# Kernel tuning notes

Hardware: AMD Instinct MI355X
Metric: run time of the kernel (lower is better)

## Reference

```python
import jax, jax.numpy as jnp
import numpy as np

NUM_EXPERTS = 8
TOP_K = 2


def setup_inputs() -> dict:
    key = jax.random.key(0)
    k1, k2, k3, k4 = jax.random.split(key, 4)
    B, T, C, E, D = 4, 2048, 2048, NUM_EXPERTS, 2048
    scale = 0.02
    return {
        "x": jax.random.normal(k1, (B, T, C), dtype=jnp.float32),
        "w_router": jax.random.normal(k2, (C, E), dtype=jnp.float32) * scale,
        "w_fc": jax.random.normal(k3, (E, C, D), dtype=jnp.float32) * scale,
        "w_proj": jax.random.normal(k4, (E, D, C), dtype=jnp.float32) * scale,
    }


def reference(x, w_router, w_fc, w_proj):
    B, T, C = x.shape
    E = w_fc.shape[0]
    x_flat = x.reshape(-1, C)                       # [N, C]
    N = x_flat.shape[0]

    router_logits = x_flat @ w_router                # [N, E]
    top_vals, top_idx = jax.lax.top_k(router_logits, TOP_K)  # [N, K]
    probs = jax.nn.softmax(top_vals, axis=-1)        # [N, K]

    # Per-token combine weight for each expert (0 if not selected).
    rows = jnp.arange(N)[:, None]                    # [N, 1]
    w_tok = jnp.zeros((N, E), dtype=x.dtype).at[rows, top_idx].add(probs)  # [N, E]

    # Dense grouped computation over experts (same math as masked loop):
    # hidden = relu(x W_fc)^2, then project and combine with routing weights.
    h = jnp.einsum('nc,ecd->ned', x_flat, w_fc)      # [N, E, D]
    h = jnp.square(jax.nn.relu(h))
    y = jnp.einsum('ned,edc->nec', h, w_proj)        # [N, E, C]
    out = jnp.einsum('nec,ne->nc', y, w_tok)         # [N, C]
    return out.reshape(B, T, C)
```

## Files before the change

kernel.cpp:

```cpp
#include <hip/hip_runtime.h>

typedef float   f32x4 __attribute__((ext_vector_type(4)));
typedef _Float16 f16x8 __attribute__((ext_vector_type(8)));
typedef short   s16x8 __attribute__((ext_vector_type(8)));
typedef short   s16x4 __attribute__((ext_vector_type(4)));
typedef unsigned short u16;

#define NTOK 8192
#define CDIM 2048
#define NEXP 8
#define NASS 16384
#define MTILES 24

#define GLOBAL_AS __attribute__((address_space(1)))
#define LDS_AS    __attribute__((address_space(3)))

__device__ __forceinline__ u16 f2h_bits(float f) {
  _Float16 h = (_Float16)f;
  union { _Float16 h; u16 u; } v;
  v.h = h;
  return v.u;
}

__global__ __launch_bounds__(256) void moe_wrt(
    const float* __restrict__ wr, float* __restrict__ wrT)
{
  const int gid = blockIdx.x * 256 + threadIdx.x;
  const int c = gid >> 3, e = gid & 7;
  wrT[e * CDIM + c] = wr[c * NEXP + e];
}

__global__ __launch_bounds__(256) void moe_router(
    const float* __restrict__ x, const float* __restrict__ wrT,
    u16* __restrict__ xh, int* __restrict__ top_idx,
    float* __restrict__ top_p, int* __restrict__ counts)
{
  const int wave = threadIdx.x >> 6, lane = threadIdx.x & 63;
  const int n = blockIdx.x * 4 + wave;
  const float* xr = x + (size_t)n * CDIM;
  u16* xhr = xh + (size_t)n * CDIM;
  float acc[NEXP] = {};
  #pragma unroll
  for (int i = 0; i < CDIM / 256; ++i) {
    const int c = i * 256 + lane * 4;
    const f32x4 xv = *(const f32x4*)(xr + c);
    s16x4 hv;
    #pragma unroll
    for (int j = 0; j < 4; ++j) hv[j] = (short)f2h_bits(xv[j]);
    *(s16x4*)(xhr + c) = hv;
    #pragma unroll
    for (int e = 0; e < NEXP; ++e) {
      const f32x4 wv = *(const f32x4*)(wrT + (size_t)e * CDIM + c);
      acc[e] += xv[0]*wv[0] + xv[1]*wv[1] + xv[2]*wv[2] + xv[3]*wv[3];
    }
  }
  #pragma unroll
  for (int off = 32; off > 0; off >>= 1) {
    #pragma unroll
    for (int e = 0; e < NEXP; ++e) acc[e] += __shfl_xor(acc[e], off);
  }
  if (lane == 0) {
    int i0 = 0; float v0 = acc[0];
    #pragma unroll
    for (int e = 1; e < NEXP; ++e) { if (acc[e] > v0) { v0 = acc[e]; i0 = e; } }
    int i1 = -1; float v1 = -3.4e38f;
    #pragma unroll
    for (int e = 0; e < NEXP; ++e) { if (e != i0 && acc[e] > v1) { v1 = acc[e]; i1 = e; } }
    const float ex = __expf(v1 - v0);
    const float p0 = 1.f / (1.f + ex);
    top_idx[n * 2 + 0] = i0; top_idx[n * 2 + 1] = i1;
    top_p[n * 2 + 0] = p0;   top_p[n * 2 + 1] = 1.f - p0;
    atomicAdd(&counts[i0], 1);
    atomicAdd(&counts[i1], 1);
  }
}

__global__ void moe_offsets(const int* __restrict__ counts,
                            int* __restrict__ offs, int* __restrict__ fill)
{
  if (threadIdx.x == 0) {
    int s = 0;
    for (int e = 0; e < NEXP; ++e) { offs[e] = s; fill[e] = s; s += counts[e]; }
    offs[NEXP] = s;
  }
}

__global__ __launch_bounds__(256) void moe_scatter(
    const int* __restrict__ top_idx, const float* __restrict__ top_p,
    int* fill, int* __restrict__ tok_s, float* __restrict__ prb_s)
{
  const int n = blockIdx.x * 256 + threadIdx.x;
  #pragma unroll
  for (int k = 0; k < 2; ++k) {
    const int e = top_idx[n * 2 + k];
    const int pos = atomicAdd(&fill[e], 1);
    tok_s[pos] = n;
    prb_s[pos] = top_p[n * 2 + k];
  }
}

__global__ __launch_bounds__(256) void moe_transpose(
    const float* __restrict__ wfc, const float* __restrict__ wpj,
    u16* __restrict__ wfcT, u16* __restrict__ wpjT)
{
  const float* src = blockIdx.z ? wpj : wfc;
  u16* dst = blockIdx.z ? wpjT : wfcT;
  const int e = blockIdx.y;
  src += (size_t)e * CDIM * CDIM;
  dst += (size_t)e * CDIM * CDIM;
  const int tr = (blockIdx.x >> 5) * 64;
  const int tc = (blockIdx.x & 31) * 64;
  __shared__ float lds[64][65];
  const int t = threadIdx.x;
  #pragma unroll
  for (int p = 0; p < 4; ++p) {
    const int r  = p * 16 + (t >> 4);
    const int c4 = (t & 15) * 4;
    const f32x4 v = *(const f32x4*)(src + (size_t)(tr + r) * CDIM + tc + c4);
    #pragma unroll
    for (int j = 0; j < 4; ++j) lds[r][c4 + j] = v[j];
  }
  __syncthreads();
  const int d  = t >> 2;
  const int cs = (t & 3) * 16;
  s16x8 o0, o1;
  #pragma unroll
  for (int j = 0; j < 8; ++j) o0[j] = (short)f2h_bits(lds[cs + j][d]);
  #pragma unroll
  for (int j = 0; j < 8; ++j) o1[j] = (short)f2h_bits(lds[cs + 8 + j][d]);
  u16* drow = dst + (size_t)(tc + d) * CDIM + tr + cs;
  *(s16x8*)(drow + 0) = o0;
  *(s16x8*)(drow + 8) = o1;
}

template<int MODE>
__global__ __launch_bounds__(512, 4) void moe_gemm8(
    const u16* __restrict__ A, const u16* __restrict__ W,
    const int* __restrict__ tok_s, const float* __restrict__ prb_s,
    const int* __restrict__ offs, u16* __restrict__ hout,
    float* __restrict__ out)
{
  const int id    = blockIdx.x;
  const int nt    = id & 7;
  const int rid   = id >> 3;
  const int e     = rid / MTILES;
  const int mtile = rid % MTILES;
  const int off0  = offs[e];
  const int Me    = offs[e + 1] - off0;
  const int m0    = mtile * 128;
  if (m0 >= Me) return;
  const int n0 = nt * 256;
  const u16* We = W + (size_t)e * CDIM * CDIM;

  __shared__ u16 As[3][128 * 32];
  __shared__ u16 Bs[3][256 * 32];

  const int t    = threadIdx.x;
  const int lane = t & 63, wv = t >> 6;
  const int wm = wv >> 2, wn = wv & 3;

  const int l     = lane;
  const int kchnk = (l & 3) ^ ((l >> 3) & 3);
  const int kelem = kchnk * 8;
  const int rloc  = 2 * (l >> 3) + ((l >> 2) & 1);
  const int rA  = wv * 16 + rloc;
  const int mrA = m0 + rA;
  const int rrA = (mrA < Me) ? mrA : (Me - 1);
  const int gaA = (MODE == 0) ? tok_s[off0 + rrA] : (off0 + rrA);
  const u16* asrc = A + (size_t)gaA * CDIM + kelem;
  const int rB0 = wv * 32 + rloc;
  const int rB1 = wv * 32 + 16 + rloc;
  const u16* bsrc0 = We + (size_t)(n0 + rB0) * CDIM + kelem;
  const u16* bsrc1 = We + (size_t)(n0 + rB1) * CDIM + kelem;

  #define STAGE(T_, bb_)                                                       \
    { const int kk_ = (T_) * 32;                                               \
      __builtin_amdgcn_global_load_lds(                                        \
          (const GLOBAL_AS void*)(asrc + kk_),                                 \
          (LDS_AS void*)&As[bb_][wv * 512], 16, 0, 0);                         \
      __builtin_amdgcn_global_load_lds(                                        \
          (const GLOBAL_AS void*)(bsrc0 + kk_),                                \
          (LDS_AS void*)&Bs[bb_][wv * 1024], 16, 0, 0);                        \
      __builtin_amdgcn_global_load_lds(                                        \
          (const GLOBAL_AS void*)(bsrc1 + kk_),                                \
          (LDS_AS void*)&Bs[bb_][wv * 1024 + 512], 16, 0, 0); }

  const int rsel     = lane & 15;
  const int g        = lane >> 4;
  const int halfline = rsel >> 1;
  const int slotx    = (((rsel & 1) * 4) + (g ^ (halfline & 3))) * 8;

  f32x4 acc[4][4] = {};

  #define COMPUTE(bb)                                                          \
    { f16x8 bv[4];                                                             \
      _Pragma("unroll")                                                        \
      for (int fn = 0; fn < 4; ++fn)                                           \
        bv[fn] = *(const f16x8*)&Bs[bb][(wn * 32 + fn * 8 + halfline) * 64 + slotx]; \
      _Pragma("unroll")                                                        \
      for (int fi = 0; fi < 4; ++fi) {                                         \
        const f16x8 av = *(const f16x8*)&As[bb][(wm * 32 + fi * 8 + halfline) * 64 + slotx]; \
        _Pragma("unroll")                                                      \
        for (int fn = 0; fn < 4; ++fn)                                         \
          acc[fi][fn] = __builtin_amdgcn_mfma_f32_16x16x32_f16(                \
              av, bv[fn], acc[fi][fn], 0, 0, 0);                               \
      } }

  STAGE(0, 0); STAGE(1, 1); STAGE(2, 2);
  int bb = 0;
  #pragma unroll 3
  for (int T = 0; T < 64; ++T) {
    if (T < 62)       { asm volatile("s_waitcnt vmcnt(6)" ::: "memory"); }
    else if (T == 62) { asm volatile("s_waitcnt vmcnt(3)" ::: "memory"); }
    else              { asm volatile("s_waitcnt vmcnt(0)" ::: "memory"); }
    __builtin_amdgcn_s_barrier();
    COMPUTE(bb);
    __builtin_amdgcn_s_barrier();
    if (T < 61) STAGE(T + 3, bb);
    bb = (bb == 2) ? 0 : bb + 1;
  }
  #undef STAGE
  #undef COMPUTE

  const int crow = g * 4;
  const int ccol = rsel;
  #pragma unroll
  for (int fi = 0; fi < 4; ++fi) {
    #pragma unroll
    for (int j = 0; j < 4; ++j) {
      const int r = m0 + wm * 64 + fi * 16 + crow + j;
      if (r >= Me) continue;
      const int s = off0 + r;
      if (MODE == 0) {
        u16* hr = hout + (size_t)s * CDIM;
        #pragma unroll
        for (int fn = 0; fn < 4; ++fn) {
          float v = acc[fi][fn][j];
          v = v > 0.f ? v * v : 0.f;
          hr[n0 + wn * 64 + fn * 16 + ccol] = f2h_bits(v);
        }
      } else {
        const float p = prb_s[s];
        float* orow = out + (size_t)tok_s[s] * CDIM;
        #pragma unroll
        for (int fn = 0; fn < 4; ++fn)
          atomicAdd(&orow[n0 + wn * 64 + fn * 16 + ccol], p * acc[fi][fn][j]);
      }
    }
  }
}

extern "C" void kernel_launch(void* const* d_in, const int* in_sizes, int n_in,
                              void* d_out, int out_size, void* d_ws, size_t ws_size,
                              hipStream_t stream)
{
  const float* x   = (const float*)d_in[0];
  const float* wr  = (const float*)d_in[1];
  const float* wfc = (const float*)d_in[2];
  const float* wpj = (const float*)d_in[3];
  float* out = (float*)d_out;
  char* ws = (char*)d_ws;

  const size_t OFF_TIDX = 256;
  const size_t OFF_TP   = OFF_TIDX + (size_t)NASS * 4;
  const size_t OFF_TOK  = OFF_TP   + (size_t)NASS * 4;
  const size_t OFF_PRB  = OFF_TOK  + (size_t)NASS * 4;
  const size_t OFF_WRT  = OFF_PRB  + (size_t)NASS * 4;
  const size_t OFF_XH   = (size_t)1 << 20;
  const size_t OFF_WFCT = OFF_XH   + (size_t)NTOK * CDIM * 2;
  const size_t OFF_WPJT = OFF_WFCT + (size_t)NEXP * CDIM * CDIM * 2;
  const size_t OFF_H    = OFF_WPJT + (size_t)NEXP * CDIM * CDIM * 2;
  const size_t NEED     = OFF_H    + (size_t)NASS * CDIM * 2;

  if (ws_size < NEED) {
    hipMemsetAsync(d_out, 0, (size_t)out_size * 4, stream);
    return;
  }

  int*   counts = (int*)(ws + 0);
  int*   offs   = (int*)(ws + 64);
  int*   fill   = (int*)(ws + 128);
  int*   tidx   = (int*)(ws + OFF_TIDX);
  float* tp     = (float*)(ws + OFF_TP);
  int*   tok    = (int*)(ws + OFF_TOK);
  float* prb    = (float*)(ws + OFF_PRB);
  float* wrT    = (float*)(ws + OFF_WRT);
  u16*   xh     = (u16*)(ws + OFF_XH);
  u16*   wfcT   = (u16*)(ws + OFF_WFCT);
  u16*   wpjT   = (u16*)(ws + OFF_WPJT);
  u16*   h      = (u16*)(ws + OFF_H);

  hipMemsetAsync(ws, 0, 256, stream);
  hipMemsetAsync(d_out, 0, (size_t)out_size * 4, stream);

  moe_wrt     <<<NEXP * CDIM / 256, 256, 0, stream>>>(wr, wrT);
  moe_router  <<<NTOK / 4, 256, 0, stream>>>(x, wrT, xh, tidx, tp, counts);
  moe_offsets <<<1, 64, 0, stream>>>(counts, offs, fill);
  moe_scatter <<<NTOK / 256, 256, 0, stream>>>(tidx, tp, fill, tok, prb);
  moe_transpose<<<dim3(1024, NEXP, 2), 256, 0, stream>>>(wfc, wpj, wfcT, wpjT);
  moe_gemm8<0><<<NEXP * 8 * MTILES, 512, 0, stream>>>(xh, wfcT, tok, nullptr, offs, h, nullptr);
  moe_gemm8<1><<<NEXP * 8 * MTILES, 512, 0, stream>>>(h,  wpjT, tok, prb,     offs, nullptr, out);
}
```

Before: 757.4 us.

## Restructure GEMM pipeline to single barrier, batch router counts, widen transpose tiles

The grouped GEMM loop now issues the next stage load right after one barrier, before computing on the current buffer. Prefetch depth drops from three stages to two, which removes the second barrier per iteration. The router processes 32 tokens per block and accumulates expert counts in shared-memory atomics, then writes them to global memory once per block. The weight transpose uses 64x128 tiles so each thread writes 32 contiguous halves. These are several independent changes to lower sync and atomic overhead, at the cost of less load latency hiding in the GEMM.

```diff
diff --git a/kernel.cpp b/kernel.cpp
--- a/kernel.cpp
+++ b/kernel.cpp
@@ -35,44 +35,51 @@
     u16* __restrict__ xh, int* __restrict__ top_idx,
     float* __restrict__ top_p, int* __restrict__ counts)
 {
+  __shared__ int scnt[NEXP];
+  if (threadIdx.x < NEXP) scnt[threadIdx.x] = 0;
+  __syncthreads();
   const int wave = threadIdx.x >> 6, lane = threadIdx.x & 63;
-  const int n = blockIdx.x * 4 + wave;
-  const float* xr = x + (size_t)n * CDIM;
-  u16* xhr = xh + (size_t)n * CDIM;
-  float acc[NEXP] = {};
-  #pragma unroll
-  for (int i = 0; i < CDIM / 256; ++i) {
-    const int c = i * 256 + lane * 4;
-    const f32x4 xv = *(const f32x4*)(xr + c);
-    s16x4 hv;
-    #pragma unroll
-    for (int j = 0; j < 4; ++j) hv[j] = (short)f2h_bits(xv[j]);
-    *(s16x4*)(xhr + c) = hv;
-    #pragma unroll
-    for (int e = 0; e < NEXP; ++e) {
-      const f32x4 wv = *(const f32x4*)(wrT + (size_t)e * CDIM + c);
-      acc[e] += xv[0]*wv[0] + xv[1]*wv[1] + xv[2]*wv[2] + xv[3]*wv[3];
-    }
-  }
-  #pragma unroll
-  for (int off = 32; off > 0; off >>= 1) {
-    #pragma unroll
-    for (int e = 0; e < NEXP; ++e) acc[e] += __shfl_xor(acc[e], off);
-  }
-  if (lane == 0) {
-    int i0 = 0; float v0 = acc[0];
-    #pragma unroll
-    for (int e = 1; e < NEXP; ++e) { if (acc[e] > v0) { v0 = acc[e]; i0 = e; } }
-    int i1 = -1; float v1 = -3.4e38f;
-    #pragma unroll
-    for (int e = 0; e < NEXP; ++e) { if (e != i0 && acc[e] > v1) { v1 = acc[e]; i1 = e; } }
-    const float ex = __expf(v1 - v0);
-    const float p0 = 1.f / (1.f + ex);
-    top_idx[n * 2 + 0] = i0; top_idx[n * 2 + 1] = i1;
-    top_p[n * 2 + 0] = p0;   top_p[n * 2 + 1] = 1.f - p0;
-    atomicAdd(&counts[i0], 1);
-    atomicAdd(&counts[i1], 1);
-  }
+  for (int i = 0; i < 8; ++i) {
+    const int n = blockIdx.x * 32 + i * 4 + wave;
+    const float* xr = x + (size_t)n * CDIM;
+    u16* xhr = xh + (size_t)n * CDIM;
+    float acc[NEXP] = {};
+    #pragma unroll
+    for (int ii = 0; ii < CDIM / 256; ++ii) {
+      const int c = ii * 256 + lane * 4;
+      const f32x4 xv = *(const f32x4*)(xr + c);
+      s16x4 hv;
+      #pragma unroll
+      for (int j = 0; j < 4; ++j) hv[j] = (short)f2h_bits(xv[j]);
+      *(s16x4*)(xhr + c) = hv;
+      #pragma unroll
+      for (int e = 0; e < NEXP; ++e) {
+        const f32x4 wv = *(const f32x4*)(wrT + (size_t)e * CDIM + c);
+        acc[e] += xv[0]*wv[0] + xv[1]*wv[1] + xv[2]*wv[2] + xv[3]*wv[3];
+      }
+    }
+    #pragma unroll
+    for (int off = 32; off > 0; off >>= 1) {
+      #pragma unroll
+      for (int e = 0; e < NEXP; ++e) acc[e] += __shfl_xor(acc[e], off);
+    }
+    if (lane == 0) {
+      int i0 = 0; float v0 = acc[0];
+      #pragma unroll
+      for (int e = 1; e < NEXP; ++e) { if (acc[e] > v0) { v0 = acc[e]; i0 = e; } }
+      int i1 = -1; float v1 = -3.4e38f;
+      #pragma unroll
+      for (int e = 0; e < NEXP; ++e) { if (e != i0 && acc[e] > v1) { v1 = acc[e]; i1 = e; } }
+      const float ex = __expf(v1 - v0);
+      const float p0 = 1.f / (1.f + ex);
+      top_idx[n * 2 + 0] = i0; top_idx[n * 2 + 1] = i1;
+      top_p[n * 2 + 0] = p0;   top_p[n * 2 + 1] = 1.f - p0;
+      atomicAdd(&scnt[i0], 1);
+      atomicAdd(&scnt[i1], 1);
+    }
+  }
+  __syncthreads();
+  if (threadIdx.x < NEXP) atomicAdd(&counts[threadIdx.x], scnt[threadIdx.x]);
 }
 
 __global__ void moe_offsets(const int* __restrict__ counts,
@@ -108,33 +115,33 @@
   const int e = blockIdx.y;
   src += (size_t)e * CDIM * CDIM;
   dst += (size_t)e * CDIM * CDIM;
-  const int tr = (blockIdx.x >> 5) * 64;
-  const int tc = (blockIdx.x & 31) * 64;
-  __shared__ float lds[64][65];
+  const int tr = (blockIdx.x >> 4) * 64;
+  const int tc = (blockIdx.x & 15) * 128;
+  __shared__ float lds[64][129];
   const int t = threadIdx.x;
   #pragma unroll
-  for (int p = 0; p < 4; ++p) {
-    const int r  = p * 16 + (t >> 4);
-    const int c4 = (t & 15) * 4;
+  for (int p = 0; p < 8; ++p) {
+    const int r  = p * 8 + (t >> 5);
+    const int c4 = (t & 31) * 4;
     const f32x4 v = *(const f32x4*)(src + (size_t)(tr + r) * CDIM + tc + c4);
     #pragma unroll
     for (int j = 0; j < 4; ++j) lds[r][c4 + j] = v[j];
   }
   __syncthreads();
-  const int d  = t >> 2;
-  const int cs = (t & 3) * 16;
-  s16x8 o0, o1;
+  const int d  = t >> 1;
+  const int ks = (t & 1) * 32;
+  u16* drow = dst + (size_t)(tc + d) * CDIM + tr + ks;
   #pragma unroll
-  for (int j = 0; j < 8; ++j) o0[j] = (short)f2h_bits(lds[cs + j][d]);
-  #pragma unroll
-  for (int j = 0; j < 8; ++j) o1[j] = (short)f2h_bits(lds[cs + 8 + j][d]);
-  u16* drow = dst + (size_t)(tc + d) * CDIM + tr + cs;
-  *(s16x8*)(drow + 0) = o0;
-  *(s16x8*)(drow + 8) = o1;
+  for (int q = 0; q < 4; ++q) {
+    s16x8 o;
+    #pragma unroll
+    for (int j = 0; j < 8; ++j) o[j] = (short)f2h_bits(lds[ks + q * 8 + j][d]);
+    *(s16x8*)(drow + q * 8) = o;
+  }
 }
 
 template<int MODE>
-__global__ __launch_bounds__(512, 4) void moe_gemm8(
+__global__ __launch_bounds__(512, 4) void moe_gemm9(
     const u16* __restrict__ A, const u16* __restrict__ W,
     const int* __restrict__ tok_s, const float* __restrict__ prb_s,
     const int* __restrict__ offs, u16* __restrict__ hout,
@@ -206,17 +213,18 @@
               av, bv[fn], acc[fi][fn], 0, 0, 0);                               \
       } }
 
-  STAGE(0, 0); STAGE(1, 1); STAGE(2, 2);
+  STAGE(0, 0); STAGE(1, 1);
   int bb = 0;
   #pragma unroll 3
   for (int T = 0; T < 64; ++T) {
-    if (T < 62)       { asm volatile("s_waitcnt vmcnt(6)" ::: "memory"); }
-    else if (T == 62) { asm volatile("s_waitcnt vmcnt(3)" ::: "memory"); }
-    else              { asm volatile("s_waitcnt vmcnt(0)" ::: "memory"); }
+    if (T < 63) { asm volatile("s_waitcnt vmcnt(3)" ::: "memory"); }
+    else        { asm volatile("s_waitcnt vmcnt(0)" ::: "memory"); }
     __builtin_amdgcn_s_barrier();
+    if (T < 62) {
+      const int b2 = (bb >= 1) ? bb - 1 : bb + 2;
+      STAGE(T + 2, b2);
+    }
     COMPUTE(bb);
-    __builtin_amdgcn_s_barrier();
-    if (T < 61) STAGE(T + 3, bb);
     bb = (bb == 2) ? 0 : bb + 1;
   }
   #undef STAGE
@@ -294,10 +302,10 @@
   hipMemsetAsync(d_out, 0, (size_t)out_size * 4, stream);
 
   moe_wrt     <<<NEXP * CDIM / 256, 256, 0, stream>>>(wr, wrT);
-  moe_router  <<<NTOK / 4, 256, 0, stream>>>(x, wrT, xh, tidx, tp, counts);
+  moe_router  <<<256, 256, 0, stream>>>(x, wrT, xh, tidx, tp, counts);
   moe_offsets <<<1, 64, 0, stream>>>(counts, offs, fill);
   moe_scatter <<<NTOK / 256, 256, 0, stream>>>(tidx, tp, fill, tok, prb);
-  moe_transpose<<<dim3(1024, NEXP, 2), 256, 0, stream>>>(wfc, wpj, wfcT, wpjT);
-  moe_gemm8<0><<<NEXP * 8 * MTILES, 512, 0, stream>>>(xh, wfcT, tok, nullptr, offs, h, nullptr);
-  moe_gemm8<1><<<NEXP * 8 * MTILES, 512, 0, stream>>>(h,  wpjT, tok, prb,     offs, nullptr, out);
-}
+  moe_transpose<<<dim3(512, NEXP, 2), 256, 0, stream>>>(wfc, wpj, wfcT, wpjT);
+  moe_gemm9<0><<<NEXP * 8 * MTILES, 512, 0, stream>>>(xh, wfcT, tok, nullptr, offs, h, nullptr);
+  moe_gemm9<1><<<NEXP * 8 * MTILES, 512, 0, stream>>>(h,  wpjT, tok, prb,     offs, nullptr, out);
+}
```

New measurement: 610.8 us. 19.4% less time.
